# Kernel optimization log

Measured on AMD Instinct MI355X. Metric: run time of the kernel, lower is better.

Reference implementation:

```python
import jax, jax.numpy as jnp
import numpy as np

B, IMG, PATCH = 32, 128, 8
D, H, L, MLP, NC = 512, 8, 8, 2048, 3
P = (IMG // PATCH) ** 2  # 256 patches
N = P + 1                # +cls token
HD = D // H


def layer_norm(x, g, b, eps=1e-5):
    mu = jnp.mean(x, -1, keepdims=True)
    var = jnp.mean((x - mu) ** 2, -1, keepdims=True)
    return (x - mu) * jax.lax.rsqrt(var + eps) * g + b


def spt(x, w, b, g, beta):
    s = 1
    shifts = [x,
              jnp.roll(x, (s, s), (2, 3)),
              jnp.roll(x, (-s, s), (2, 3)),
              jnp.roll(x, (s, -s), (2, 3)),
              jnp.roll(x, (-s, -s), (2, 3))]
    xs = jnp.concatenate(shifts, axis=1)  # (B,5,H,W)
    y = jax.lax.conv_general_dilated(
        xs, w, (PATCH, PATCH), 'VALID',
        dimension_numbers=('NCHW', 'OIHW', 'NCHW')) + b[None, :, None, None]
    tok = y.reshape(y.shape[0], D, -1).transpose(0, 2, 1)  # (B,P,D)
    return layer_norm(tok, g, beta)


def block(tok, p):
    ln1g, ln1b, qkvw, qkvb, projw, projb, temp, ln2g, ln2b, w1, b1, w2, b2 = p
    x = layer_norm(tok, ln1g, ln1b)
    qkv = (x @ qkvw + qkvb).reshape(x.shape[0], N, 3, H, HD)
    q = jnp.transpose(qkv[:, :, 0], (0, 2, 1, 3))  # (B,H,N,HD)
    k = jnp.transpose(qkv[:, :, 1], (0, 2, 1, 3))
    v = jnp.transpose(qkv[:, :, 2], (0, 2, 1, 3))
    attn = jnp.einsum('bhnd,bhmd->bhnm', q, k) * temp[None, :, None, None]
    attn = jnp.where(jnp.eye(N, dtype=bool)[None, None], -jnp.inf, attn)
    attn = jax.nn.softmax(attn, -1)
    o = jnp.einsum('bhnm,bhmd->bhnd', attn, v)
    o = jnp.transpose(o, (0, 2, 1, 3)).reshape(x.shape[0], N, D)
    tok = tok + o @ projw + projb
    y = layer_norm(tok, ln2g, ln2b)
    y = jax.nn.gelu(y @ w1 + b1, approximate=False) @ w2 + b2
    return tok + y


def setup_inputs() -> dict:
    key = jax.random.key(0)
    ks = jax.random.split(key, 16)
    sc = 0.02
    inp = dict(
        image=jax.random.uniform(ks[0], (B, 1, IMG, IMG), jnp.float32),
        ssw=jax.random.normal(ks[1], (D, 5, PATCH, PATCH), jnp.float32) * sc,
        ssb=jnp.zeros((D,), jnp.float32),
        ssg=jnp.ones((D,), jnp.float32),
        ssbeta=jnp.zeros((D,), jnp.float32),
        sow=jax.random.normal(ks[2], (D, 5, PATCH, PATCH), jnp.float32) * sc,
        sob=jnp.zeros((D,), jnp.float32),
        sog=jnp.ones((D,), jnp.float32),
        sobeta=jnp.zeros((D,), jnp.float32),
        fw=jax.random.normal(ks[3], (2 * D, D), jnp.float32) * sc,
        fb=jnp.zeros((D,), jnp.float32),
        cls_token=jax.random.normal(ks[4], (1, 1, D), jnp.float32) * sc,
        pos_embed=jax.random.normal(ks[5], (1, N, D), jnp.float32) * sc,
        ln1g=jnp.ones((L, D), jnp.float32),
        ln1b=jnp.zeros((L, D), jnp.float32),
        qkvw=jax.random.normal(ks[6], (L, D, 3 * D), jnp.float32) * sc,
        qkvb=jnp.zeros((L, 3 * D), jnp.float32),
        projw=jax.random.normal(ks[7], (L, D, D), jnp.float32) * sc,
        projb=jnp.zeros((L, D), jnp.float32),
        temp=jnp.ones((L, H), jnp.float32) / np.sqrt(HD),
        ln2g=jnp.ones((L, D), jnp.float32),
        ln2b=jnp.zeros((L, D), jnp.float32),
        w1=jax.random.normal(ks[8], (L, D, MLP), jnp.float32) * sc,
        b1=jnp.zeros((L, MLP), jnp.float32),
        w2=jax.random.normal(ks[9], (L, MLP, D), jnp.float32) * sc,
        b2=jnp.zeros((L, D), jnp.float32),
        ng=jnp.ones((D,), jnp.float32),
        nb=jnp.zeros((D,), jnp.float32),
        hw=jax.random.normal(ks[10], (D, NC), jnp.float32) * sc,
        hb=jnp.zeros((NC,), jnp.float32),
    )
    return inp


def reference(image, ssw, ssb, ssg, ssbeta, sow, sob, sog, sobeta, fw, fb,
              cls_token, pos_embed, ln1g, ln1b, qkvw, qkvb, projw, projb,
              temp, ln2g, ln2b, w1, b1, w2, b2, ng, nb, hw, hb):
    # InverseLensLayer is undefined in the source repo snippet: identity
    source = image
    src_tok = spt(source, ssw, ssb, ssg, ssbeta)   # (B,P,D)
    orig_tok = spt(image, sow, sob, sog, sobeta)   # (B,P,D)
    comb = jnp.concatenate([src_tok, orig_tok], -1)
    gate = jax.nn.sigmoid(comb @ fw + fb)
    fused = gate * src_tok + (1.0 - gate) * orig_tok
    cls = jnp.broadcast_to(cls_token, (image.shape[0], 1, D))
    tokens = jnp.concatenate([cls, fused], axis=1) + pos_embed  # (B,N,D)

    def body(tok, p):
        return block(tok, p), None

    params = (ln1g, ln1b, qkvw, qkvb, projw, projb, temp,
              ln2g, ln2b, w1, b1, w2, b2)
    tokens, _ = jax.lax.scan(body, tokens, params)
    cls_out = layer_norm(tokens[:, 0], ng, nb)
    logits = cls_out @ hw + hb
    return logits
```

## Files before the change

kernel.cpp:

```cpp
#include <hip/hip_runtime.h>
#include <math.h>

constexpr int B_ = 32, D_ = 512, H_ = 8, L_ = 8, MLP_ = 2048, NC_ = 3;
constexpr int P_ = 256;
constexpr int N_ = 257;
constexpr int HD_ = 64;
constexpr int BP_ = B_ * P_;
constexpr int BN_ = B_ * N_;
constexpr int MP_ = 8320;
constexpr int KP_ = 320;

enum { EPI_BIAS = 0, EPI_RES = 1, EPI_GELU = 2 };

using bf16x8 = __attribute__((ext_vector_type(8))) short;
using f32x4  = __attribute__((ext_vector_type(4))) float;

__device__ __forceinline__ float b2f(unsigned short u) {
    return __uint_as_float(((unsigned)u) << 16);
}
__device__ __forceinline__ unsigned short f2b(float f) {
    unsigned u = __float_as_uint(f);
    unsigned r = (u + 0x7FFFu + ((u >> 16) & 1u)) >> 16;
    return (unsigned short)r;
}

__device__ __forceinline__ void gld_lds16(const void* g, void* l) {
    __builtin_amdgcn_global_load_lds(
        (const __attribute__((address_space(1))) void*)g,
        (__attribute__((address_space(3))) void*)l, 16, 0, 0);
}

__global__ void im2col_k(const float* __restrict__ img,
                         unsigned short* __restrict__ X) {
    int idx = blockIdx.x * 256 + threadIdx.x;
    if (idx >= BP_ * KP_) return;
    int r = idx / KP_, j = idx % KP_;
    int b = r >> 8, p = r & 255;
    int py = p >> 4, px = p & 15;
    int c = j >> 6, kk = j & 63;
    int ky = kk >> 3, kx = kk & 7;
    const int dy[5] = {0, 1, -1, 1, -1};
    const int dx[5] = {0, 1, 1, -1, -1};
    int yy = (py * 8 + ky - dy[c] + 128) & 127;
    int xx = (px * 8 + kx - dx[c] + 128) & 127;
    X[idx] = f2b(img[b * 16384 + yy * 128 + xx]);
}

__global__ __launch_bounds__(256) void castT_k(const float* __restrict__ in,
                                               unsigned short* __restrict__ out,
                                               int K, int N) {
    __shared__ float t[32][33];
    size_t loff = (size_t)blockIdx.z * K * N;
    int k0 = blockIdx.x * 32, n0 = blockIdx.y * 32;
    int tx = threadIdx.x & 31, ty = threadIdx.x >> 5;
    for (int i = ty; i < 32; i += 8)
        t[i][tx] = in[loff + (size_t)(k0 + i) * N + n0 + tx];
    __syncthreads();
    for (int i = ty; i < 32; i += 8)
        out[loff + (size_t)(n0 + i) * K + k0 + tx] = f2b(t[tx][i]);
}

__global__ void cast_k(const float* __restrict__ in,
                       unsigned short* __restrict__ out, int n) {
    int idx = blockIdx.x * 256 + threadIdx.x;
    if (idx < n) out[idx] = f2b(in[idx]);
}

__global__ __launch_bounds__(256) void gemm_bf16_k(
    const unsigned short* __restrict__ A, const unsigned short* __restrict__ Bt,
    const float* __restrict__ bias, const float* __restrict__ res,
    float* __restrict__ outF, unsigned short* __restrict__ outB,
    int Nn, int K, int epi) {
    constexpr int BK = 32;
    __shared__ unsigned short As[128 * BK];
    __shared__ unsigned short Bs[128 * BK];
    int tid = threadIdx.x, lane = tid & 63;
    int wave = tid >> 6;
    int wrow = (wave >> 1) * 64, wcol = (wave & 1) * 64;
    size_t bm = (size_t)blockIdx.y * 128, bn = (size_t)blockIdx.x * 128;
    const unsigned short* Ab = A + bm * K;
    const unsigned short* Bb = Bt + bn * K;

    f32x4 acc[4][4] = {};
    int quad = lane >> 4, col = lane & 15;
    int q8 = quad * 8;

    for (int k0 = 0; k0 < K; k0 += BK) {
#pragma unroll
        for (int it = 0; it < 2; ++it) {
            int c = it * 256 + tid;
            int row = c >> 2, cb = (c & 3) * 8;
            gld_lds16(Ab + (size_t)row * K + k0 + cb, (char*)As + c * 16);
            gld_lds16(Bb + (size_t)row * K + k0 + cb, (char*)Bs + c * 16);
        }
        __syncthreads();
        bf16x8 af[4], bfr[4];
#pragma unroll
        for (int i = 0; i < 4; ++i) {
            af[i]  = *(const bf16x8*)&As[(wrow + i * 16 + col) * BK + q8];
            bfr[i] = *(const bf16x8*)&Bs[(wcol + i * 16 + col) * BK + q8];
        }
#pragma unroll
        for (int mi = 0; mi < 4; ++mi)
#pragma unroll
            for (int ni = 0; ni < 4; ++ni)
                acc[mi][ni] = __builtin_amdgcn_mfma_f32_16x16x32_bf16(
                    af[mi], bfr[ni], acc[mi][ni], 0, 0, 0);
        __syncthreads();
    }

#pragma unroll
    for (int mi = 0; mi < 4; ++mi) {
#pragma unroll
        for (int ni = 0; ni < 4; ++ni) {
            size_t gm0 = bm + wrow + mi * 16 + quad * 4;
            size_t gn = bn + wcol + ni * 16 + col;
            float bs = bias ? bias[gn] : 0.f;
#pragma unroll
            for (int r = 0; r < 4; ++r) {
                size_t o = (gm0 + r) * Nn + gn;
                float v = acc[mi][ni][r] + bs;
                if (epi == EPI_GELU)
                    v = 0.5f * v * (1.f + erff(v * 0.70710678118654752f));
                else if (epi == EPI_RES)
                    v += res[o];
                if (outF) outF[o] = v;
                if (outB) outB[o] = f2b(v);
            }
        }
    }
}

__global__ __launch_bounds__(256) void ln_k(
    const float* __restrict__ in, float* __restrict__ outF,
    unsigned short* __restrict__ outB, const float* __restrict__ g,
    const float* __restrict__ be, long instride, long ofs, long obs) {
    __shared__ float red[256];
    int row = blockIdx.x;
    const float* x = in + (size_t)row * instride;
    int t = threadIdx.x;
    float v0 = x[t], v1 = x[t + 256];
    red[t] = v0 + v1;
    __syncthreads();
    for (int s = 128; s > 0; s >>= 1) {
        if (t < s) red[t] += red[t + s];
        __syncthreads();
    }
    float mu = red[0] * (1.f / 512.f);
    __syncthreads();
    float d0 = v0 - mu, d1 = v1 - mu;
    red[t] = d0 * d0 + d1 * d1;
    __syncthreads();
    for (int s = 128; s > 0; s >>= 1) {
        if (t < s) red[t] += red[t + s];
        __syncthreads();
    }
    float rs = rsqrtf(red[0] * (1.f / 512.f) + 1e-5f);
    float y0 = d0 * rs * g[t] + be[t];
    float y1 = d1 * rs * g[t + 256] + be[t + 256];
    if (outF) {
        float* y = outF + (size_t)row * ofs;
        y[t] = y0; y[t + 256] = y1;
    }
    if (outB) {
        unsigned short* y = outB + (size_t)row * obs;
        y[t] = f2b(y0); y[t + 256] = f2b(y1);
    }
}

__global__ void assemble_k(const float* __restrict__ gatelin,
                           const float* __restrict__ src,
                           const float* __restrict__ orig,
                           const float* __restrict__ cls,
                           const float* __restrict__ pos,
                           float* __restrict__ tokens) {
    int idx = blockIdx.x * 256 + threadIdx.x;
    if (idx >= B_ * N_ * D_) return;
    int d = idx & 511;
    int bn = idx >> 9;
    int b = bn / N_, n = bn % N_;
    float v;
    if (n == 0) {
        v = cls[d];
    } else {
        int r = b * 256 + (n - 1);
        float gl = gatelin[r * 512 + d];
        float g = 1.f / (1.f + expf(-gl));
        v = g * src[r * 512 + d] + (1.f - g) * orig[r * 512 + d];
    }
    tokens[idx] = v + pos[n * 512 + d];
}

__global__ __launch_bounds__(256) void attn_fused_k(
    const unsigned short* __restrict__ qkv, const float* __restrict__ temp,
    unsigned short* __restrict__ obuf) {
    __shared__ __align__(16) unsigned short Vt[64][296];
    __shared__ __align__(16) unsigned short Ps[4][16][40];
    int blk = blockIdx.x;
    int bh = blk >> 1, half = blk & 1;
    int b = bh >> 3, h = bh & 7;
    int tid = threadIdx.x, lane = tid & 63, wave = tid >> 6;
    int quad = lane >> 4, cid = lane & 15;
    const unsigned short* qb = qkv + (size_t)(b * N_) * 1536 + h * 64;

    for (int idx = tid; idx < 257 * 8; idx += 256) {
        int n = idx >> 3, c = idx & 7;
        uint4 u = *(const uint4*)(qb + (size_t)n * 1536 + 1024 + c * 8);
        const unsigned short* e = (const unsigned short*)&u;
#pragma unroll
        for (int j = 0; j < 8; ++j) Vt[c * 8 + j][n] = e[j];
    }
    for (int idx = tid; idx < 64 * 31; idx += 256)
        Vt[idx / 31][257 + idx % 31] = 0;
    __syncthreads();

    float tmp = temp[h];
    int qt_end = half ? 17 : 9;
    for (int qt = half * 9 + wave; qt < qt_end; qt += 4) {
        int qrow_l = qt * 16 + cid;
        if (qrow_l > 256) qrow_l = 256;
        bf16x8 aq0 = *(const bf16x8*)(qb + (size_t)qrow_l * 1536 + quad * 8);
        bf16x8 aq1 = *(const bf16x8*)(qb + (size_t)qrow_l * 1536 + 32 + quad * 8);

        f32x4 s[18];
#pragma unroll 1
        for (int t = 0; t < 17; ++t) {
            int krow = t * 16 + cid;
            if (krow > 256) krow = 256;
            const unsigned short* kp = qb + 512 + (size_t)krow * 1536;
            bf16x8 bk0 = *(const bf16x8*)(kp + quad * 8);
            bf16x8 bk1 = *(const bf16x8*)(kp + 32 + quad * 8);
            f32x4 a = {0.f, 0.f, 0.f, 0.f};
            a = __builtin_amdgcn_mfma_f32_16x16x32_bf16(aq0, bk0, a, 0, 0, 0);
            a = __builtin_amdgcn_mfma_f32_16x16x32_bf16(aq1, bk1, a, 0, 0, 0);
            s[t] = a;
        }
        float mx[4] = {-1e30f, -1e30f, -1e30f, -1e30f};
#pragma unroll
        for (int t = 0; t < 17; ++t) {
            int col = t * 16 + cid;
#pragma unroll
            for (int r = 0; r < 4; ++r) {
                int row = qt * 16 + quad * 4 + r;
                float v = s[t][r] * tmp;
                if (col == row || col >= 257) v = -1e30f;
                s[t][r] = v;
                mx[r] = fmaxf(mx[r], v);
            }
        }
        s[17] = f32x4{-1e30f, -1e30f, -1e30f, -1e30f};
#pragma unroll
        for (int m = 1; m < 16; m <<= 1)
#pragma unroll
            for (int r = 0; r < 4; ++r)
                mx[r] = fmaxf(mx[r], __shfl_xor(mx[r], m));
        float sum[4] = {0.f, 0.f, 0.f, 0.f};
#pragma unroll
        for (int t = 0; t < 18; ++t)
#pragma unroll
            for (int r = 0; r < 4; ++r) {
                float e = __expf(s[t][r] - mx[r]);
                float ef = b2f(f2b(e));
                s[t][r] = ef;
                sum[r] += ef;
            }
#pragma unroll
        for (int m = 1; m < 16; m <<= 1)
#pragma unroll
            for (int r = 0; r < 4; ++r) sum[r] += __shfl_xor(sum[r], m);
        float inv[4];
#pragma unroll
        for (int r = 0; r < 4; ++r) inv[r] = 1.f / sum[r];

        f32x4 o[4] = {};
#pragma unroll 1
        for (int kt = 0; kt < 9; ++kt) {
#pragma unroll
            for (int hh = 0; hh < 2; ++hh) {
                int t = kt * 2 + hh;
#pragma unroll
                for (int r = 0; r < 4; ++r)
                    Ps[wave][quad * 4 + r][hh * 16 + cid] = f2b(s[t][r]);
            }
            bf16x8 ap = *(const bf16x8*)&Ps[wave][cid][quad * 8];
#pragma unroll
            for (int dt = 0; dt < 4; ++dt) {
                bf16x8 bv =
                    *(const bf16x8*)&Vt[dt * 16 + cid][kt * 32 + quad * 8];
                o[dt] = __builtin_amdgcn_mfma_f32_16x16x32_bf16(ap, bv, o[dt],
                                                                0, 0, 0);
            }
        }
#pragma unroll
        for (int dt = 0; dt < 4; ++dt)
#pragma unroll
            for (int r = 0; r < 4; ++r) {
                int row = qt * 16 + quad * 4 + r;
                if (row < N_)
                    obuf[(size_t)(b * N_ + row) * 512 + h * 64 + dt * 16 +
                         cid] = f2b(o[dt][r] * inv[r]);
            }
    }
}

__global__ void head_k(const float* __restrict__ cls_out,
                       const float* __restrict__ hw,
                       const float* __restrict__ hb, float* __restrict__ out) {
    int t = threadIdx.x;
    if (t >= B_ * NC_) return;
    int b = t / NC_, c = t % NC_;
    float acc = hb[c];
    for (int d = 0; d < D_; ++d) acc += cls_out[b * D_ + d] * hw[d * NC_ + c];
    out[t] = acc;
}

extern "C" void kernel_launch(void* const* d_in, const int* in_sizes, int n_in,
                              void* d_out, int out_size, void* d_ws,
                              size_t ws_size, hipStream_t stream) {
    const float* image     = (const float*)d_in[0];
    const float* ssw       = (const float*)d_in[1];
    const float* ssb       = (const float*)d_in[2];
    const float* ssg       = (const float*)d_in[3];
    const float* ssbeta    = (const float*)d_in[4];
    const float* sow       = (const float*)d_in[5];
    const float* sob       = (const float*)d_in[6];
    const float* sog       = (const float*)d_in[7];
    const float* sobeta    = (const float*)d_in[8];
    const float* fw        = (const float*)d_in[9];
    const float* fb        = (const float*)d_in[10];
    const float* cls_token = (const float*)d_in[11];
    const float* pos_embed = (const float*)d_in[12];
    const float* ln1g      = (const float*)d_in[13];
    const float* ln1b      = (const float*)d_in[14];
    const float* qkvw      = (const float*)d_in[15];
    const float* qkvb      = (const float*)d_in[16];
    const float* projw     = (const float*)d_in[17];
    const float* projb     = (const float*)d_in[18];
    const float* temp      = (const float*)d_in[19];
    const float* ln2g      = (const float*)d_in[20];
    const float* ln2b      = (const float*)d_in[21];
    const float* w1        = (const float*)d_in[22];
    const float* b1        = (const float*)d_in[23];
    const float* w2        = (const float*)d_in[24];
    const float* b2        = (const float*)d_in[25];
    const float* ng        = (const float*)d_in[26];
    const float* nb        = (const float*)d_in[27];
    const float* hw        = (const float*)d_in[28];
    const float* hb        = (const float*)d_in[29];
    float* out = (float*)d_out;

    char* w = (char*)d_ws;
    size_t off = 0;
    float* tokens = (float*)w;                           off += (size_t)MP_ * 512 * 4;
    unsigned short* qkvw_t = (unsigned short*)(w + off); off += (size_t)8 * 1536 * 512 * 2;
    unsigned short* projw_t = (unsigned short*)(w + off); off += (size_t)8 * 512 * 512 * 2;
    unsigned short* w1_t = (unsigned short*)(w + off);   off += (size_t)8 * 2048 * 512 * 2;
    unsigned short* w2_t = (unsigned short*)(w + off);   off += (size_t)8 * 512 * 2048 * 2;
    unsigned short* fw_t = (unsigned short*)(w + off);   off += (size_t)512 * 1024 * 2;
    unsigned short* sswb = (unsigned short*)(w + off);   off += (size_t)512 * 320 * 2;
    unsigned short* sowb = (unsigned short*)(w + off);   off += (size_t)512 * 320 * 2;
    char* S = w + off;

    unsigned short* Xb   = (unsigned short*)S;
    float* srct          = (float*)(S + 5242880);
    float* origt         = (float*)(S + 5242880 + 16777216);
    unsigned short* comb = (unsigned short*)(S + 5242880 + 2 * 16777216);
    float* gatelin       = (float*)(S + 5242880 + 3 * 16777216);

    unsigned short* xbuf = (unsigned short*)S;
    unsigned short* qkvB = (unsigned short*)(S + 8519680);
    unsigned short* obuf = (unsigned short*)(S + 8519680 + 25559040);
    unsigned short* hbuf = (unsigned short*)(S + 8519680 + 25559040 + 8519680);
    float* cls_out       = (float*)(S + 8519680 + 25559040 + 8519680 + 34078720);

    castT_k<<<dim3(16, 48, 8), 256, 0, stream>>>(qkvw, qkvw_t, 512, 1536);
    castT_k<<<dim3(16, 16, 8), 256, 0, stream>>>(projw, projw_t, 512, 512);
    castT_k<<<dim3(16, 64, 8), 256, 0, stream>>>(w1, w1_t, 512, 2048);
    castT_k<<<dim3(64, 16, 8), 256, 0, stream>>>(w2, w2_t, 2048, 512);
    castT_k<<<dim3(32, 16, 1), 256, 0, stream>>>(fw, fw_t, 1024, 512);
    cast_k<<<640, 256, 0, stream>>>(ssw, sswb, 512 * 320);
    cast_k<<<640, 256, 0, stream>>>(sow, sowb, 512 * 320);

    im2col_k<<<(BP_ * KP_ + 255) / 256, 256, 0, stream>>>(image, Xb);
    dim3 gspt(4, 64);
    gemm_bf16_k<<<gspt, 256, 0, stream>>>(Xb, sswb, ssb, nullptr, srct, nullptr,
                                          512, KP_, EPI_BIAS);
    ln_k<<<BP_, 256, 0, stream>>>(srct, srct, comb, ssg, ssbeta, 512, 512, 1024);
    gemm_bf16_k<<<gspt, 256, 0, stream>>>(Xb, sowb, sob, nullptr, origt, nullptr,
                                          512, KP_, EPI_BIAS);
    ln_k<<<BP_, 256, 0, stream>>>(origt, origt, comb + 512, sog, sobeta, 512,
                                  512, 1024);
    gemm_bf16_k<<<gspt, 256, 0, stream>>>(comb, fw_t, fb, nullptr, gatelin,
                                          nullptr, 512, 1024, EPI_BIAS);
    assemble_k<<<(B_ * N_ * D_ + 255) / 256, 256, 0, stream>>>(
        gatelin, srct, origt, cls_token, pos_embed, tokens);

    dim3 gqkv(12, 65), gproj(4, 65), gfc1(16, 65);
    for (int l = 0; l < L_; ++l) {
        const float* l1g = ln1g + l * D_;
        const float* l1b = ln1b + l * D_;
        const unsigned short* qw = qkvw_t + (size_t)l * 1536 * 512;
        const float* qb  = qkvb + (size_t)l * 3 * D_;
        const unsigned short* pw = projw_t + (size_t)l * 512 * 512;
        const float* pb  = projb + (size_t)l * D_;
        const float* tp  = temp + l * H_;
        const float* l2g = ln2g + l * D_;
        const float* l2b = ln2b + l * D_;
        const unsigned short* w1l = w1_t + (size_t)l * 2048 * 512;
        const float* b1l = b1 + (size_t)l * MLP_;
        const unsigned short* w2l = w2_t + (size_t)l * 512 * 2048;
        const float* b2l = b2 + (size_t)l * D_;

        ln_k<<<BN_, 256, 0, stream>>>(tokens, nullptr, xbuf, l1g, l1b, 512, 0,
                                      512);
        gemm_bf16_k<<<gqkv, 256, 0, stream>>>(xbuf, qw, qb, nullptr, nullptr,
                                              qkvB, 1536, 512, EPI_BIAS);
        attn_fused_k<<<B_ * H_ * 2, 256, 0, stream>>>(qkvB, tp, obuf);
        gemm_bf16_k<<<gproj, 256, 0, stream>>>(obuf, pw, pb, tokens, tokens,
                                               nullptr, 512, 512, EPI_RES);
        ln_k<<<BN_, 256, 0, stream>>>(tokens, nullptr, xbuf, l2g, l2b, 512, 0,
                                      512);
        gemm_bf16_k<<<gfc1, 256, 0, stream>>>(xbuf, w1l, b1l, nullptr, nullptr,
                                              hbuf, 2048, 512, EPI_GELU);
        gemm_bf16_k<<<gproj, 256, 0, stream>>>(hbuf, w2l, b2l, tokens, tokens,
                                               nullptr, 512, 2048, EPI_RES);
    }

    ln_k<<<B_, 256, 0, stream>>>(tokens, cls_out, nullptr, ng, nb,
                                 (long)N_ * 512, 512, 0);
    head_k<<<1, 128, 0, stream>>>(cls_out, hw, hb, out);
}
```

Before: 2.861 ms.

## Precompute V transpose in separate kernel and spread attention query tiles across blocks

```diff
diff --git a/kernel.cpp b/kernel.cpp
--- a/kernel.cpp
+++ b/kernel.cpp
@@ -9,6 +9,7 @@
 constexpr int BN_ = B_ * N_;
 constexpr int MP_ = 8320;
 constexpr int KP_ = 320;
+constexpr int NV_ = 288;
 
 enum { EPI_BIAS = 0, EPI_RES = 1, EPI_GELU = 2 };
 
@@ -191,116 +192,141 @@
     tokens[idx] = v + pos[n * 512 + d];
 }
 
+__global__ __launch_bounds__(256) void vT_k(const unsigned short* __restrict__ qkv,
+                                            unsigned short* __restrict__ Vt_g) {
+    __shared__ unsigned short t[64][72];
+    int bh = blockIdx.x, nt = blockIdx.y;
+    int b = bh >> 3, h = bh & 7;
+    int n0 = nt * 64;
+    const unsigned short* vb = qkv + (size_t)(b * N_) * 1536 + 1024 + h * 64;
+    int tid = threadIdx.x;
+    for (int idx = tid; idx < 64 * 8; idx += 256) {
+        int n = idx >> 3, c = idx & 7;
+        int gn = n0 + n;
+        uint4 u = {0, 0, 0, 0};
+        if (gn < N_) u = *(const uint4*)(vb + (size_t)gn * 1536 + c * 8);
+        *(uint4*)&t[n][c * 8] = u;
+    }
+    __syncthreads();
+    for (int idx = tid; idx < 64 * 8; idx += 256) {
+        int d = idx >> 3, j = idx & 7;
+        if (n0 + j * 8 >= NV_) continue;
+        unsigned short tmp[8];
+#pragma unroll
+        for (int e = 0; e < 8; ++e) tmp[e] = t[j * 8 + e][d];
+        *(uint4*)&Vt_g[((size_t)bh * 64 + d) * NV_ + n0 + j * 8] =
+            *(uint4*)tmp;
+    }
+}
+
 __global__ __launch_bounds__(256) void attn_fused_k(
-    const unsigned short* __restrict__ qkv, const float* __restrict__ temp,
+    const unsigned short* __restrict__ qkv,
+    const unsigned short* __restrict__ Vt_g, const float* __restrict__ temp,
     unsigned short* __restrict__ obuf) {
-    __shared__ __align__(16) unsigned short Vt[64][296];
     __shared__ __align__(16) unsigned short Ps[4][16][40];
-    int blk = blockIdx.x;
-    int bh = blk >> 1, half = blk & 1;
+    int bh = blockIdx.x;
     int b = bh >> 3, h = bh & 7;
     int tid = threadIdx.x, lane = tid & 63, wave = tid >> 6;
     int quad = lane >> 4, cid = lane & 15;
+    int qt = blockIdx.y * 4 + wave;
+    if (qt > 16) return;
     const unsigned short* qb = qkv + (size_t)(b * N_) * 1536 + h * 64;
-
-    for (int idx = tid; idx < 257 * 8; idx += 256) {
-        int n = idx >> 3, c = idx & 7;
-        uint4 u = *(const uint4*)(qb + (size_t)n * 1536 + 1024 + c * 8);
-        const unsigned short* e = (const unsigned short*)&u;
-#pragma unroll
-        for (int j = 0; j < 8; ++j) Vt[c * 8 + j][n] = e[j];
-    }
-    for (int idx = tid; idx < 64 * 31; idx += 256)
-        Vt[idx / 31][257 + idx % 31] = 0;
-    __syncthreads();
-
+    const unsigned short* kb = qb + 512;
+    const unsigned short* vt = Vt_g + (size_t)bh * 64 * NV_;
     float tmp = temp[h];
-    int qt_end = half ? 17 : 9;
-    for (int qt = half * 9 + wave; qt < qt_end; qt += 4) {
-        int qrow_l = qt * 16 + cid;
-        if (qrow_l > 256) qrow_l = 256;
-        bf16x8 aq0 = *(const bf16x8*)(qb + (size_t)qrow_l * 1536 + quad * 8);
-        bf16x8 aq1 = *(const bf16x8*)(qb + (size_t)qrow_l * 1536 + 32 + quad * 8);
-
-        f32x4 s[18];
-#pragma unroll 1
-        for (int t = 0; t < 17; ++t) {
-            int krow = t * 16 + cid;
-            if (krow > 256) krow = 256;
-            const unsigned short* kp = qb + 512 + (size_t)krow * 1536;
-            bf16x8 bk0 = *(const bf16x8*)(kp + quad * 8);
-            bf16x8 bk1 = *(const bf16x8*)(kp + 32 + quad * 8);
-            f32x4 a = {0.f, 0.f, 0.f, 0.f};
-            a = __builtin_amdgcn_mfma_f32_16x16x32_bf16(aq0, bk0, a, 0, 0, 0);
-            a = __builtin_amdgcn_mfma_f32_16x16x32_bf16(aq1, bk1, a, 0, 0, 0);
-            s[t] = a;
-        }
-        float mx[4] = {-1e30f, -1e30f, -1e30f, -1e30f};
-#pragma unroll
-        for (int t = 0; t < 17; ++t) {
-            int col = t * 16 + cid;
-#pragma unroll
-            for (int r = 0; r < 4; ++r) {
-                int row = qt * 16 + quad * 4 + r;
-                float v = s[t][r] * tmp;
-                if (col == row || col >= 257) v = -1e30f;
-                s[t][r] = v;
-                mx[r] = fmaxf(mx[r], v);
-            }
-        }
-        s[17] = f32x4{-1e30f, -1e30f, -1e30f, -1e30f};
-#pragma unroll
-        for (int m = 1; m < 16; m <<= 1)
+
+    int qrow = qt * 16 + cid;
+    if (qrow > 256) qrow = 256;
+    bf16x8 aq0 = *(const bf16x8*)(qb + (size_t)qrow * 1536 + quad * 8);
+    bf16x8 aq1 = *(const bf16x8*)(qb + (size_t)qrow * 1536 + 32 + quad * 8);
+
+    f32x4 s[18];
+#pragma unroll 4
+    for (int t = 0; t < 16; ++t) {
+        const unsigned short* kp = kb + (size_t)(t * 16 + cid) * 1536 + quad * 8;
+        bf16x8 bk0 = *(const bf16x8*)kp;
+        bf16x8 bk1 = *(const bf16x8*)(kp + 32);
+        f32x4 a = {0.f, 0.f, 0.f, 0.f};
+        a = __builtin_amdgcn_mfma_f32_16x16x32_bf16(aq0, bk0, a, 0, 0, 0);
+        a = __builtin_amdgcn_mfma_f32_16x16x32_bf16(aq1, bk1, a, 0, 0, 0);
+        s[t] = a;
+    }
+    {
+        int krow = 256 + cid;
+        if (krow > 256) krow = 256;
+        const unsigned short* kp = kb + (size_t)krow * 1536 + quad * 8;
+        bf16x8 bk0 = *(const bf16x8*)kp;
+        bf16x8 bk1 = *(const bf16x8*)(kp + 32);
+        f32x4 a = {0.f, 0.f, 0.f, 0.f};
+        a = __builtin_amdgcn_mfma_f32_16x16x32_bf16(aq0, bk0, a, 0, 0, 0);
+        a = __builtin_amdgcn_mfma_f32_16x16x32_bf16(aq1, bk1, a, 0, 0, 0);
+        s[16] = a;
+    }
+
+    float mx[4] = {-1e30f, -1e30f, -1e30f, -1e30f};
+#pragma unroll
+    for (int t = 0; t < 17; ++t) {
+        int col = t * 16 + cid;
+#pragma unroll
+        for (int r = 0; r < 4; ++r) {
+            int row = qt * 16 + quad * 4 + r;
+            float v = s[t][r] * tmp;
+            if (col == row || col >= 257) v = -1e30f;
+            s[t][r] = v;
+            mx[r] = fmaxf(mx[r], v);
+        }
+    }
+    s[17] = f32x4{-1e30f, -1e30f, -1e30f, -1e30f};
+#pragma unroll
+    for (int m = 1; m < 16; m <<= 1)
+#pragma unroll
+        for (int r = 0; r < 4; ++r) mx[r] = fmaxf(mx[r], __shfl_xor(mx[r], m));
+    float sum[4] = {0.f, 0.f, 0.f, 0.f};
+#pragma unroll
+    for (int t = 0; t < 18; ++t)
+#pragma unroll
+        for (int r = 0; r < 4; ++r) {
+            float e = __expf(s[t][r] - mx[r]);
+            float ef = b2f(f2b(e));
+            s[t][r] = ef;
+            sum[r] += ef;
+        }
+#pragma unroll
+    for (int m = 1; m < 16; m <<= 1)
+#pragma unroll
+        for (int r = 0; r < 4; ++r) sum[r] += __shfl_xor(sum[r], m);
+    float inv[4];
+#pragma unroll
+    for (int r = 0; r < 4; ++r) inv[r] = 1.f / sum[r];
+
+    f32x4 o[4] = {};
+#pragma unroll 3
+    for (int kt = 0; kt < 9; ++kt) {
+#pragma unroll
+        for (int hh = 0; hh < 2; ++hh) {
+            int t = kt * 2 + hh;
 #pragma unroll
             for (int r = 0; r < 4; ++r)
-                mx[r] = fmaxf(mx[r], __shfl_xor(mx[r], m));
-        float sum[4] = {0.f, 0.f, 0.f, 0.f};
-#pragma unroll
-        for (int t = 0; t < 18; ++t)
-#pragma unroll
-            for (int r = 0; r < 4; ++r) {
-                float e = __expf(s[t][r] - mx[r]);
-                float ef = b2f(f2b(e));
-                s[t][r] = ef;
-                sum[r] += ef;
-            }
-#pragma unroll
-        for (int m = 1; m < 16; m <<= 1)
-#pragma unroll
-            for (int r = 0; r < 4; ++r) sum[r] += __shfl_xor(sum[r], m);
-        float inv[4];
-#pragma unroll
-        for (int r = 0; r < 4; ++r) inv[r] = 1.f / sum[r];
-
-        f32x4 o[4] = {};
-#pragma unroll 1
-        for (int kt = 0; kt < 9; ++kt) {
-#pragma unroll
-            for (int hh = 0; hh < 2; ++hh) {
-                int t = kt * 2 + hh;
-#pragma unroll
-                for (int r = 0; r < 4; ++r)
-                    Ps[wave][quad * 4 + r][hh * 16 + cid] = f2b(s[t][r]);
-            }
-            bf16x8 ap = *(const bf16x8*)&Ps[wave][cid][quad * 8];
-#pragma unroll
-            for (int dt = 0; dt < 4; ++dt) {
-                bf16x8 bv =
-                    *(const bf16x8*)&Vt[dt * 16 + cid][kt * 32 + quad * 8];
-                o[dt] = __builtin_amdgcn_mfma_f32_16x16x32_bf16(ap, bv, o[dt],
-                                                                0, 0, 0);
-            }
-        }
-#pragma unroll
-        for (int dt = 0; dt < 4; ++dt)
-#pragma unroll
-            for (int r = 0; r < 4; ++r) {
-                int row = qt * 16 + quad * 4 + r;
-                if (row < N_)
-                    obuf[(size_t)(b * N_ + row) * 512 + h * 64 + dt * 16 +
-                         cid] = f2b(o[dt][r] * inv[r]);
-            }
-    }
+                Ps[wave][quad * 4 + r][hh * 16 + cid] = f2b(s[t][r]);
+        }
+        bf16x8 ap = *(const bf16x8*)&Ps[wave][cid][quad * 8];
+#pragma unroll
+        for (int dt = 0; dt < 4; ++dt) {
+            bf16x8 bv = *(const bf16x8*)(vt + (size_t)(dt * 16 + cid) * NV_ +
+                                         kt * 32 + quad * 8);
+            o[dt] =
+                __builtin_amdgcn_mfma_f32_16x16x32_bf16(ap, bv, o[dt], 0, 0, 0);
+        }
+    }
+#pragma unroll
+    for (int dt = 0; dt < 4; ++dt)
+#pragma unroll
+        for (int r = 0; r < 4; ++r) {
+            int row = qt * 16 + quad * 4 + r;
+            if (row < N_)
+                obuf[(size_t)(b * N_ + row) * 512 + h * 64 + dt * 16 + cid] =
+                    f2b(o[dt][r] * inv[r]);
+        }
 }
 
 __global__ void head_k(const float* __restrict__ cls_out,
@@ -371,7 +397,10 @@
     unsigned short* qkvB = (unsigned short*)(S + 8519680);
     unsigned short* obuf = (unsigned short*)(S + 8519680 + 25559040);
     unsigned short* hbuf = (unsigned short*)(S + 8519680 + 25559040 + 8519680);
-    float* cls_out       = (float*)(S + 8519680 + 25559040 + 8519680 + 34078720);
+    unsigned short* vt_g = (unsigned short*)(S + 8519680 + 25559040 + 8519680 +
+                                             34078720);
+    float* cls_out = (float*)(S + 8519680 + 25559040 + 8519680 + 34078720 +
+                              9437184);
 
     castT_k<<<dim3(16, 48, 8), 256, 0, stream>>>(qkvw, qkvw_t, 512, 1536);
     castT_k<<<dim3(16, 16, 8), 256, 0, stream>>>(projw, projw_t, 512, 512);
@@ -415,7 +444,8 @@
                                       512);
         gemm_bf16_k<<<gqkv, 256, 0, stream>>>(xbuf, qw, qb, nullptr, nullptr,
                                               qkvB, 1536, 512, EPI_BIAS);
-        attn_fused_k<<<B_ * H_ * 2, 256, 0, stream>>>(qkvB, tp, obuf);
+        vT_k<<<dim3(256, 5), 256, 0, stream>>>(qkvB, vt_g);
+        attn_fused_k<<<dim3(256, 5), 256, 0, stream>>>(qkvB, vt_g, tp, obuf);
         gemm_bf16_k<<<gproj, 256, 0, stream>>>(obuf, pw, pb, tokens, tokens,
                                                nullptr, 512, 512, EPI_RES);
         ln_k<<<BN_, 256, 0, stream>>>(tokens, nullptr, xbuf, l2g, l2b, 512, 0,
```

Result: no change. 2.899 ms (+1.3%).
